# Performance work log

Measured on AMD Instinct MI355X. Metric: run time of the kernel, lower is better.

The kernel has to match this reference:

```python
import jax, jax.numpy as jnp
import numpy as np

B, C_IN, C_OUT, E, H, W = 64, 384, 384, 8, 28, 28


def setup_inputs() -> dict:
    key = jax.random.key(0)
    k1, k2, k3 = jax.random.split(key, 3)
    x = jax.random.normal(k1, (B, C_IN, H, W), dtype=jnp.float32)
    routing_weights = jax.random.uniform(k2, (B, E), dtype=jnp.float32)
    # kaiming_normal_(mode='fan_out') per expert: std = sqrt(2 / fan_out), fan_out = out_channels * 1 * 1
    std = float(np.sqrt(2.0 / C_OUT))
    weight = jax.random.normal(k3, (E, C_OUT, C_IN), dtype=jnp.float32) * std
    return {"x": x, "routing_weights": routing_weights, "weight": weight}


def reference(x, routing_weights, weight):
    # Per-sample aggregated 1x1 conv weights: [b, c_out, c_in]
    agg = jnp.einsum('be,eoi->boi', routing_weights, weight)
    # Per-sample channel mixing (1x1 conv with groups=b == batched GEMM)
    out = jnp.einsum('boi,bihw->bohw', agg, x)
    return out
```

## Files before the change

### kernel.cpp

```cpp
#include <hip/hip_runtime.h>
#include <cstdint>

#define B_   64
#define CI_  384
#define CO_  384
#define HW_  784
#define E_   8

typedef unsigned short ushort_t;
typedef unsigned int   uint_t;

typedef __attribute__((ext_vector_type(8))) short bf16x8;
typedef __attribute__((ext_vector_type(4))) float f32x4;

__device__ __forceinline__ ushort_t f2bf_rne(float f) {
  uint_t u = __builtin_bit_cast(uint_t, f);
  u += 0x7fffu + ((u >> 16) & 1u);
  return (ushort_t)(u >> 16);
}

__device__ __forceinline__ uint_t pack_bf16_trunc(float f0, float f1) {
  return __builtin_amdgcn_perm(__builtin_bit_cast(uint_t, f1),
                               __builtin_bit_cast(uint_t, f0),
                               0x07060302u);
}

__global__ __launch_bounds__(256) void agg_kernel(const float* __restrict__ rw,
                                                  const float* __restrict__ w,
                                                  ushort_t* __restrict__ agg) {
  __shared__ float r[B_ * E_];
  const int tid = threadIdx.x;
  r[tid]       = rw[tid];
  r[tid + 256] = rw[tid + 256];
  const int base = blockIdx.x * 512 + tid * 2;
  float2 wv[E_];
#pragma unroll
  for (int e = 0; e < E_; ++e)
    wv[e] = *(const float2*)&w[e * (CO_ * CI_) + base];
  __syncthreads();
  const int b0 = blockIdx.y * 16;
#pragma unroll 4
  for (int bi = 0; bi < 16; ++bi) {
    const int b = b0 + bi;
    float ax = 0.f, ay = 0.f;
#pragma unroll
    for (int e = 0; e < E_; ++e) {
      const float rv = r[b * E_ + e];
      ax += rv * wv[e].x;
      ay += rv * wv[e].y;
    }
    const uint_t v = (uint_t)f2bf_rne(ax) | ((uint_t)f2bf_rne(ay) << 16);
    *(uint_t*)&agg[(size_t)b * (CO_ * CI_) + base] = v;
  }
}

#define BM 128
#define BN 128
#define BK 32
#define KIT (CI_ / BK)
#define BS_STRIDE 40

__global__ __launch_bounds__(256) void moe_gemm(const float* __restrict__ X,
                                                const ushort_t* __restrict__ Agg,
                                                float* __restrict__ Out) {
  __shared__ __align__(16) ushort_t As[BM * BK];
  __shared__ __align__(16) ushort_t Bs[BN * BS_STRIDE];

  const int tid  = threadIdx.x;
  const int lane = tid & 63;
  const int wave = tid >> 6;
  const int wm = wave & 1, wn = wave >> 1;

  const int bx = blockIdx.x;
  const int by = blockIdx.y;
  const int bg  = by / 21;
  const int rem = by - bg * 21;
  const int mt  = rem / 7;
  const int nt  = rem - mt * 7;
  const int b   = bg * 8 + bx;

  const ushort_t* Ab = Agg + (size_t)b * CO_ * CI_ + mt * BM * CI_;
  const float*    Xb = X   + (size_t)b * CI_ * HW_;

  const int sn  = tid & 127;
  const int sk4 = (tid >> 7) * 4;
  const int gn  = nt * BN + sn;
  const int gnc = gn < HW_ ? gn : (HW_ - 1);
  const float* Xcol = Xb + gnc;

  f32x4 acc[4][4];
#pragma unroll
  for (int i = 0; i < 4; ++i)
#pragma unroll
    for (int j = 0; j < 4; ++j)
      acc[i][j] = (f32x4)0.f;

  const int l15 = lane & 15;
  const int lq  = lane >> 4;
  const int xqA = lq ^ ((l15 >> 1) & 3);

  const int sm0 = tid >> 2,           sq0 = (tid & 3) ^ ((tid >> 3) & 3);
  const int sm1 = (tid + 256) >> 2,   sq1 = (tid & 3) ^ (((tid + 256) >> 3) & 3);

  for (int kk = 0; kk < KIT; ++kk) {
    const int k0 = kk * BK;
    {
      const ushort_t* src0 = Ab + sm0 * CI_ + k0 + sq0 * 8;
      __builtin_amdgcn_global_load_lds(
          (const __attribute__((address_space(1))) uint_t*)src0,
          (__attribute__((address_space(3))) uint_t*)&As[tid * 8], 16, 0, 0);
      const ushort_t* src1 = Ab + sm1 * CI_ + k0 + sq1 * 8;
      __builtin_amdgcn_global_load_lds(
          (const __attribute__((address_space(1))) uint_t*)src1,
          (__attribute__((address_space(3))) uint_t*)&As[(tid + 256) * 8], 16, 0, 0);
    }
#pragma unroll
    for (int j = 0; j < 4; ++j) {
      const int kl = j * 8 + sk4;
      const float* p = Xcol + (size_t)(k0 + kl) * HW_;
      const float v0 = p[0], v1 = p[HW_], v2 = p[2 * HW_], v3 = p[3 * HW_];
      const uint_t lo = pack_bf16_trunc(v0, v1);
      const uint_t hi = pack_bf16_trunc(v2, v3);
      *(uint2*)&Bs[sn * BS_STRIDE + kl] = make_uint2(lo, hi);
    }
    __syncthreads();
    bf16x8 a[4], bb[4];
#pragma unroll
    for (int mf = 0; mf < 4; ++mf) {
      const int m = wm * 64 + mf * 16 + l15;
      a[mf] = *(const bf16x8*)&As[(m * 4 + xqA) * 8];
    }
#pragma unroll
    for (int nf = 0; nf < 4; ++nf)
      bb[nf] = *(const bf16x8*)&Bs[(wn * 64 + nf * 16 + l15) * BS_STRIDE + lq * 8];
#pragma unroll
    for (int mf = 0; mf < 4; ++mf)
#pragma unroll
      for (int nf = 0; nf < 4; ++nf)
        acc[mf][nf] = __builtin_amdgcn_mfma_f32_16x16x32_bf16(a[mf], bb[nf],
                                                              acc[mf][nf], 0, 0, 0);
    __syncthreads();
  }

  float* Ob = Out + (size_t)b * CO_ * HW_;
#pragma unroll
  for (int mf = 0; mf < 4; ++mf) {
#pragma unroll
    for (int nf = 0; nf < 4; ++nf) {
      const int n = nt * BN + wn * 64 + nf * 16 + l15;
      if (n < HW_) {
        const int mbase = mt * BM + wm * 64 + mf * 16 + lq * 4;
#pragma unroll
        for (int r = 0; r < 4; ++r)
          Ob[(size_t)(mbase + r) * HW_ + n] = acc[mf][nf][r];
      }
    }
  }
}

extern "C" void kernel_launch(void* const* d_in, const int* in_sizes, int n_in,
                              void* d_out, int out_size, void* d_ws, size_t ws_size,
                              hipStream_t stream) {
  const float* x  = (const float*)d_in[0];
  const float* rw = (const float*)d_in[1];
  const float* w  = (const float*)d_in[2];
  float* out = (float*)d_out;
  ushort_t* agg = (ushort_t*)d_ws;

  agg_kernel<<<dim3((CO_ * CI_) / 512, 4), 256, 0, stream>>>(rw, w, agg);
  moe_gemm<<<dim3(8, 168), 256, 0, stream>>>(x, agg, out);
}
```

Measured before the change: 175.9 us.

## Double-buffer GEMM LDS tiles and prefetch next K-slice during MFMA

Adds double-buffered As/Bs shared tiles. The next K-slice's A (global_load_lds) and X values (held in registers) are issued before the current slice's MFMAs, and the X values are packed to bf16 into the other buffer after compute. This leaves one barrier per iteration and lets global latency overlap with matrix math. The B tile also switches from a padded stride to an XOR-swizzled 32-wide layout read with two 8-byte loads. The cost is more LDS, 16 extra registers per thread, and possibly lower occupancy.

```diff
diff --git a/kernel.cpp b/kernel.cpp
--- a/kernel.cpp
+++ b/kernel.cpp
@@ -10,8 +10,9 @@
 typedef unsigned short ushort_t;
 typedef unsigned int   uint_t;
 
-typedef __attribute__((ext_vector_type(8))) short bf16x8;
-typedef __attribute__((ext_vector_type(4))) float f32x4;
+typedef __attribute__((ext_vector_type(8))) short  bf16x8;
+typedef __attribute__((ext_vector_type(4))) float  f32x4;
+typedef __attribute__((ext_vector_type(4))) uint_t uint32x4;
 
 __device__ __forceinline__ ushort_t f2bf_rne(float f) {
   uint_t u = __builtin_bit_cast(uint_t, f);
@@ -58,13 +59,12 @@
 #define BN 128
 #define BK 32
 #define KIT (CI_ / BK)
-#define BS_STRIDE 40
 
 __global__ __launch_bounds__(256) void moe_gemm(const float* __restrict__ X,
                                                 const ushort_t* __restrict__ Agg,
                                                 float* __restrict__ Out) {
-  __shared__ __align__(16) ushort_t As[BM * BK];
-  __shared__ __align__(16) ushort_t Bs[BN * BS_STRIDE];
+  __shared__ __align__(16) ushort_t As[2][BM * BK];
+  __shared__ __align__(16) ushort_t Bs[2][BN * BK];
 
   const int tid  = threadIdx.x;
   const int lane = tid & 63;
@@ -87,59 +87,92 @@
   const int gn  = nt * BN + sn;
   const int gnc = gn < HW_ ? gn : (HW_ - 1);
   const float* Xcol = Xb + gnc;
-
-  f32x4 acc[4][4];
-#pragma unroll
-  for (int i = 0; i < 4; ++i)
-#pragma unroll
-    for (int j = 0; j < 4; ++j)
-      acc[i][j] = (f32x4)0.f;
+  const int swz = (sn >> 1) & 7;
+
+  const int sm0 = tid >> 2,           sq0 = (tid & 3) ^ ((tid >> 3) & 3);
+  const int sm1 = (tid + 256) >> 2,   sq1 = (tid & 3) ^ (((tid + 256) >> 3) & 3);
 
   const int l15 = lane & 15;
   const int lq  = lane >> 4;
   const int xqA = lq ^ ((l15 >> 1) & 3);
 
-  const int sm0 = tid >> 2,           sq0 = (tid & 3) ^ ((tid >> 3) & 3);
-  const int sm1 = (tid + 256) >> 2,   sq1 = (tid & 3) ^ (((tid + 256) >> 3) & 3);
-
+  f32x4 acc[4][4];
+#pragma unroll
+  for (int i = 0; i < 4; ++i)
+#pragma unroll
+    for (int j = 0; j < 4; ++j)
+      acc[i][j] = (f32x4)0.f;
+
+  float bv[16];
+
+  auto stage_a = [&](int k0, int bsel) {
+    const ushort_t* src0 = Ab + sm0 * CI_ + k0 + sq0 * 8;
+    __builtin_amdgcn_global_load_lds(
+        (const __attribute__((address_space(1))) uint_t*)src0,
+        (__attribute__((address_space(3))) uint_t*)&As[bsel][tid * 8], 16, 0, 0);
+    const ushort_t* src1 = Ab + sm1 * CI_ + k0 + sq1 * 8;
+    __builtin_amdgcn_global_load_lds(
+        (const __attribute__((address_space(1))) uint_t*)src1,
+        (__attribute__((address_space(3))) uint_t*)&As[bsel][(tid + 256) * 8], 16, 0, 0);
+  };
+  auto load_b = [&](int k0) {
+#pragma unroll
+    for (int j = 0; j < 4; ++j) {
+      const float* p = Xcol + (size_t)(k0 + j * 8 + sk4) * HW_;
+#pragma unroll
+      for (int c = 0; c < 4; ++c)
+        bv[j * 4 + c] = p[c * HW_];
+    }
+  };
+  auto pack_b = [&](int bsel) {
+#pragma unroll
+    for (int j = 0; j < 4; ++j) {
+      const int c  = 2 * j + (sk4 >> 2);
+      const int pc = c ^ swz;
+      const uint_t lo = pack_bf16_trunc(bv[j * 4 + 0], bv[j * 4 + 1]);
+      const uint_t hi = pack_bf16_trunc(bv[j * 4 + 2], bv[j * 4 + 3]);
+      *(uint2*)&Bs[bsel][sn * 32 + pc * 4] = make_uint2(lo, hi);
+    }
+  };
+
+  stage_a(0, 0);
+  load_b(0);
+  pack_b(0);
+
+  int buf = 0;
   for (int kk = 0; kk < KIT; ++kk) {
-    const int k0 = kk * BK;
-    {
-      const ushort_t* src0 = Ab + sm0 * CI_ + k0 + sq0 * 8;
-      __builtin_amdgcn_global_load_lds(
-          (const __attribute__((address_space(1))) uint_t*)src0,
-          (__attribute__((address_space(3))) uint_t*)&As[tid * 8], 16, 0, 0);
-      const ushort_t* src1 = Ab + sm1 * CI_ + k0 + sq1 * 8;
-      __builtin_amdgcn_global_load_lds(
-          (const __attribute__((address_space(1))) uint_t*)src1,
-          (__attribute__((address_space(3))) uint_t*)&As[(tid + 256) * 8], 16, 0, 0);
-    }
-#pragma unroll
-    for (int j = 0; j < 4; ++j) {
-      const int kl = j * 8 + sk4;
-      const float* p = Xcol + (size_t)(k0 + kl) * HW_;
-      const float v0 = p[0], v1 = p[HW_], v2 = p[2 * HW_], v3 = p[3 * HW_];
-      const uint_t lo = pack_bf16_trunc(v0, v1);
-      const uint_t hi = pack_bf16_trunc(v2, v3);
-      *(uint2*)&Bs[sn * BS_STRIDE + kl] = make_uint2(lo, hi);
-    }
     __syncthreads();
+    const int nb = buf ^ 1;
+    if (kk + 1 < KIT) {
+      stage_a((kk + 1) * BK, nb);
+      load_b((kk + 1) * BK);
+    }
     bf16x8 a[4], bb[4];
 #pragma unroll
     for (int mf = 0; mf < 4; ++mf) {
       const int m = wm * 64 + mf * 16 + l15;
-      a[mf] = *(const bf16x8*)&As[(m * 4 + xqA) * 8];
-    }
-#pragma unroll
-    for (int nf = 0; nf < 4; ++nf)
-      bb[nf] = *(const bf16x8*)&Bs[(wn * 64 + nf * 16 + l15) * BS_STRIDE + lq * 8];
+      a[mf] = *(const bf16x8*)&As[buf][(m * 4 + xqA) * 8];
+    }
+#pragma unroll
+    for (int nf = 0; nf < 4; ++nf) {
+      const int rn = wn * 64 + nf * 16 + l15;
+      const int h  = (rn >> 1) & 7;
+      const int p0 = (2 * lq) ^ h;
+      const uint2 lo = *(const uint2*)&Bs[buf][rn * 32 + p0 * 4];
+      const uint2 hi = *(const uint2*)&Bs[buf][rn * 32 + (p0 ^ 1) * 4];
+      uint32x4 u;
+      u[0] = lo.x; u[1] = lo.y; u[2] = hi.x; u[3] = hi.y;
+      bb[nf] = __builtin_bit_cast(bf16x8, u);
+    }
 #pragma unroll
     for (int mf = 0; mf < 4; ++mf)
 #pragma unroll
       for (int nf = 0; nf < 4; ++nf)
         acc[mf][nf] = __builtin_amdgcn_mfma_f32_16x16x32_bf16(a[mf], bb[nf],
                                                               acc[mf][nf], 0, 0, 0);
-    __syncthreads();
+    if (kk + 1 < KIT)
+      pack_b(nb);
+    buf = nb;
   }
 
   float* Ob = Out + (size_t)b * CO_ * HW_;
```

Result: no change. 176.7 us (+0.4%).
